# Kernel tuning notes

Hardware: AMD Instinct MI355X
Metric: run time of the kernel (lower is better)

The kernel has to match this reference:

```python
import jax, jax.numpy as jnp
import numpy as np

B, NODES, IN_DIM, OUT_DIM, CAPS, K, NUM_ROUTE = 32, 512, 256, 128, 16, 5, 3

def squash(s):
    # s: [..., out]; scale = |s|^2/(1+|s|^2), direction s/(|s|+eps)
    sn = jnp.sum(s * s, axis=-1, keepdims=True)
    return (sn / (1.0 + sn)) * s / (jnp.sqrt(sn) + 1e-8)

def setup_inputs() -> dict:
    key = jax.random.key(0)
    k1, k2, k3, k4 = jax.random.split(key, 4)
    return {
        "x": jax.random.normal(k1, (B, NODES, IN_DIM), jnp.float32),
        "contribution": jax.random.normal(k2, (B, NODES), jnp.float32),
        "W": jax.random.normal(k3, (K, IN_DIM, OUT_DIM), jnp.float32),
        "alpha": jax.random.normal(k4, (NODES, CAPS, K), jnp.float32),
    }

def reference(x, contribution, W, alpha):
    # per-node, per-capsule transform: sum_k alpha[n,c,k] * W[k,i,o] -> [nodes, caps, in, out]
    Wn = jnp.einsum('nck,kio->ncio', alpha, W)
    # prediction vectors u_hat: [B, caps, nodes, out]
    u_hat = jnp.einsum('bni,ncio->bcno', x, Wn)
    u_det = jax.lax.stop_gradient(u_hat)
    # routing logits b init from (detached) contribution: [B, caps, nodes, 1]
    b = jnp.broadcast_to(
        jax.lax.stop_gradient(contribution)[:, None, :, None],
        (x.shape[0], CAPS, x.shape[1], 1))
    for _ in range(NUM_ROUTE):
        c = jax.nn.softmax(b, axis=1)              # over capsule axis
        v = squash(jnp.sum(c * u_det, axis=2))     # [B, caps, out]
        b = b + jnp.einsum('bcno,bco->bcn', u_det, v)[..., None]
    c = jax.nn.softmax(b, axis=1)
    s = jnp.sum(c * u_hat, axis=2)                 # [B, caps, out] (non-detached)
    return squash(s)
```

## Files before the change

### kernel.cpp

```cpp
#include <hip/hip_runtime.h>
#include <math.h>

#define B_ 32
#define NODES_ 512
#define IN_ 256
#define OUT_ 128
#define CAPS_ 16
#define KW_ 5
#define M_ (B_*NODES_)
#define N_ (KW_*OUT_)
#define NCH 32

typedef __attribute__((ext_vector_type(8))) short short8;
typedef __attribute__((ext_vector_type(4))) float f32x4;

#define Y_BOFF   0
#define L_BOFF   41943040
#define V_BOFF   42991616
#define SP_BOFF  43253760
#define BT_SZ    (N_*IN_*2)

#define YPAD 648
#define APAD 84

__device__ __forceinline__ float b2f(unsigned short u) {
  union { unsigned int i; float f; } c; c.i = ((unsigned int)u) << 16; return c.f;
}
__device__ __forceinline__ unsigned short f2b(float f) {
  union { float f; unsigned int i; } c; c.f = f;
  unsigned int u = c.i;
  u += 0x7fffu + ((u >> 16) & 1u);
  return (unsigned short)(u >> 16);
}
__device__ __forceinline__ void async_load16(const void* g, void* l) {
  __builtin_amdgcn_global_load_lds(
      (const __attribute__((address_space(1))) unsigned int*)g,
      (__attribute__((address_space(3))) unsigned int*)l, 16, 0, 0);
}

__global__ __launch_bounds__(256) void conv_w(const float* __restrict__ W,
                                              unsigned short* __restrict__ bThi,
                                              unsigned short* __restrict__ bTlo) {
  int n = blockIdx.x;
  int i = threadIdx.x;
  int k = n >> 7, o = n & 127;
  float v = W[((size_t)k*IN_ + i)*OUT_ + o];
  unsigned short h = f2b(v);
  size_t dst = ((size_t)(i >> 3)*N_ + n)*8 + (i & 7);
  bThi[dst] = h;
  bTlo[dst] = f2b(v - b2f(h));
}

__global__ __launch_bounds__(512) void gemm_fn(const float* __restrict__ x,
                                               const unsigned short* __restrict__ bThi,
                                               const unsigned short* __restrict__ bTlo,
                                               float* __restrict__ y) {
  __shared__ float A_lds[8*64*4];
  __shared__ short Bh_lds[4*640*8];
  __shared__ short Bl_lds[4*640*8];
  const int t    = threadIdx.x;
  const int w    = t >> 6;
  const int lane = t & 63;
  const int lrow = lane & 15;
  const int lk   = lane >> 4;
  const int m0   = blockIdx.x * 64;
  const int wn0  = w * 80;
  const int arow = t >> 3;
  const int ac4  = t & 7;

  f32x4 acc[4][5];
  #pragma unroll
  for (int i=0;i<4;++i)
    #pragma unroll
    for (int j=0;j<5;++j) acc[i][j] = (f32x4){0.f,0.f,0.f,0.f};

  for (int kbi = 0; kbi < 8; ++kbi) {
    const int kb = kbi*32;
    const unsigned short* bh_src = bThi + (size_t)kbi*4*N_*8;
    const unsigned short* bl_src = bTlo + (size_t)kbi*4*N_*8;
    #pragma unroll
    for (int q=0; q<5; ++q) {
      int db = q*512 + w*64;
      async_load16(bh_src + (size_t)(db + lane)*8, &Bh_lds[db*8]);
      async_load16(bl_src + (size_t)(db + lane)*8, &Bl_lds[db*8]);
    }
    {
      float4 av = *(const float4*)(x + (size_t)(m0 + arow)*IN_ + kb + ac4*4);
      *(float4*)&A_lds[((ac4*64) + arow)*4] = av;
    }
    __syncthreads();

    short8 ah[4], al[4];
    #pragma unroll
    for (int mi=0; mi<4; ++mi) {
      int row = mi*16 + lrow;
      f32x4 a0 = *(const f32x4*)&A_lds[((2*lk  )*64 + row)*4];
      f32x4 a1 = *(const f32x4*)&A_lds[((2*lk+1)*64 + row)*4];
      #pragma unroll
      for (int j=0; j<8; ++j) {
        float f = (j < 4) ? a0[j] : a1[j-4];
        unsigned short h = f2b(f);
        ah[mi][j] = (short)h;
        al[mi][j] = (short)f2b(f - b2f(h));
      }
    }
    #pragma unroll
    for (int ni=0; ni<5; ++ni) {
      int nb = wn0 + ni*16 + lrow;
      short8 bh = *(const short8*)&Bh_lds[(lk*N_ + nb)*8];
      short8 bl = *(const short8*)&Bl_lds[(lk*N_ + nb)*8];
      #pragma unroll
      for (int mi=0; mi<4; ++mi) {
        acc[mi][ni] = __builtin_amdgcn_mfma_f32_16x16x32_bf16(bh, ah[mi], acc[mi][ni], 0, 0, 0);
        acc[mi][ni] = __builtin_amdgcn_mfma_f32_16x16x32_bf16(bh, al[mi], acc[mi][ni], 0, 0, 0);
        acc[mi][ni] = __builtin_amdgcn_mfma_f32_16x16x32_bf16(bl, ah[mi], acc[mi][ni], 0, 0, 0);
      }
    }
    __syncthreads();
  }

  #pragma unroll
  for (int mi=0; mi<4; ++mi) {
    int m = m0 + mi*16 + lrow;
    #pragma unroll
    for (int ni=0; ni<5; ++ni) {
      int nb = wn0 + ni*16 + lk*4;
      float4 o = {acc[mi][ni][0], acc[mi][ni][1], acc[mi][ni][2], acc[mi][ni][3]};
      *(float4*)(y + (size_t)m*N_ + nb) = o;
    }
  }
}

__global__ __launch_bounds__(256) void route_step(const float* __restrict__ y,
                                                  const float* __restrict__ alpha,
                                                  const float* __restrict__ contrib,
                                                  float* __restrict__ logits,
                                                  const float* __restrict__ vin,
                                                  float* __restrict__ s_part,
                                                  int mode) {
  __shared__ __align__(16) float sh_y[16*YPAD];
  __shared__ __align__(16) float sh_v[16*132];
  __shared__ __align__(16) float sh_alpha[16*APAD];
  __shared__ float sh_logit[16][16];

  const int t  = threadIdx.x;
  const int ch = blockIdx.x;
  const int b  = blockIdx.y;
  const int n0 = ch*16;

  const float* ybase = y + ((size_t)(b*NODES_ + n0))*N_;
  float4 yst[10];
  #pragma unroll
  for (int q=0; q<10; ++q) yst[q] = *(const float4*)(ybase + (size_t)(t + q*256)*4);
  #pragma unroll
  for (int q=0; q<10; ++q) {
    int flat = (t + q*256)*4;
    int nd   = flat / 640;
    int rem  = flat - nd*640;
    *(float4*)&sh_y[nd*YPAD + rem] = yst[q];
  }
  const float* abase = alpha + (size_t)n0*CAPS_*KW_;
  for (int i = t; i < 320; i += 256) {
    float4 av = *(const float4*)(abase + i*4);
    int flat = i*4;
    int nd   = flat / 80;
    int rem  = flat - nd*80;
    *(float4*)&sh_alpha[nd*APAD + rem] = av;
  }
  if (mode >= 1) {
    const float* vbase = vin + (size_t)b*CAPS_*OUT_;
    #pragma unroll
    for (int q=0; q<2; ++q) {
      int flat = (t + q*256)*4;
      int c = flat >> 7, o = flat & 127;
      float4 vv = *(const float4*)(vbase + flat);
      *(float4*)&sh_v[c*132 + o] = vv;
    }
    int nd = t & 15, cap = t >> 4;
    sh_logit[nd][cap] = logits[((size_t)b*CAPS_ + cap)*NODES_ + n0 + nd];
  } else {
    int nd = t >> 4, cap = t & 15;
    logits[((size_t)b*CAPS_ + cap)*NODES_ + n0 + nd] = contrib[(size_t)b*NODES_ + n0 + nd];
  }
  __syncthreads();

  if (mode >= 1) {
    const int node = t >> 4, s = t & 15;
    float ar[16][5];
    #pragma unroll
    for (int c=0;c<16;++c)
      #pragma unroll
      for (int k=0;k<5;++k) ar[c][k] = sh_alpha[node*APAD + c*5 + k];
    float acc16[16];
    #pragma unroll
    for (int c=0;c<16;++c) acc16[c] = 0.f;
    const float* yb = &sh_y[node*YPAD];
    #pragma unroll
    for (int j=0;j<8;++j) {
      int o = s + 16*j;
      float y0=yb[o], y1=yb[128+o], y2=yb[256+o], y3=yb[384+o], y4=yb[512+o];
      #pragma unroll
      for (int c=0;c<16;++c) {
        float u = ar[c][0]*y0 + ar[c][1]*y1 + ar[c][2]*y2 + ar[c][3]*y3 + ar[c][4]*y4;
        acc16[c] += u * sh_v[c*132 + o];
      }
    }
    #pragma unroll
    for (int c=0;c<16;++c) {
      acc16[c] += __shfl_xor(acc16[c], 1, 64);
      acc16[c] += __shfl_xor(acc16[c], 2, 64);
      acc16[c] += __shfl_xor(acc16[c], 4, 64);
      acc16[c] += __shfl_xor(acc16[c], 8, 64);
    }
    float mine = 0.f;
    #pragma unroll
    for (int c=0;c<16;++c) mine = (s == c) ? acc16[c] : mine;
    float newl = sh_logit[node][s] + mine;
    sh_logit[node][s] = newl;
    logits[((size_t)b*CAPS_ + s)*NODES_ + n0 + node] = newl;
    __syncthreads();
    if (t < 16) {
      int nd = t;
      float m = -1e30f;
      #pragma unroll
      for (int c=0;c<16;++c) m = fmaxf(m, sh_logit[nd][c]);
      float ssum = 0.f;
      float e[16];
      #pragma unroll
      for (int c=0;c<16;++c) { e[c] = __expf(sh_logit[nd][c]-m); ssum += e[c]; }
      float inv = 1.f/ssum;
      #pragma unroll
      for (int c=0;c<16;++c) sh_logit[nd][c] = e[c]*inv;
    }
  } else {
    int nd = t >> 4, cap = t & 15;
    sh_logit[nd][cap] = 1.f/16.f;
  }
  __syncthreads();

  float* spb = s_part + ((size_t)(b*NCH + ch))*CAPS_*OUT_;
  #pragma unroll
  for (int sl=0; sl<2; ++sl) {
    int slot = t + sl*256;
    int c  = slot & 15;
    int o  = (slot >> 4) * 4;
    float4 acc = {0.f,0.f,0.f,0.f};
    #pragma unroll 4
    for (int nd=0; nd<16; ++nd) {
      const float* al = &sh_alpha[nd*APAD + c*5];
      float a0=al[0],a1=al[1],a2=al[2],a3=al[3],a4=al[4];
      const float* yb = &sh_y[nd*YPAD + o];
      float4 y0 = *(const float4*)(yb);
      float4 y1 = *(const float4*)(yb + 128);
      float4 y2 = *(const float4*)(yb + 256);
      float4 y3 = *(const float4*)(yb + 384);
      float4 y4 = *(const float4*)(yb + 512);
      float cw = sh_logit[nd][c];
      acc.x += cw*(a0*y0.x + a1*y1.x + a2*y2.x + a3*y3.x + a4*y4.x);
      acc.y += cw*(a0*y0.y + a1*y1.y + a2*y2.y + a3*y3.y + a4*y4.y);
      acc.z += cw*(a0*y0.z + a1*y1.z + a2*y2.z + a3*y3.z + a4*y4.z);
      acc.w += cw*(a0*y0.w + a1*y1.w + a2*y2.w + a3*y3.w + a4*y4.w);
    }
    *(float4*)(spb + c*OUT_ + o) = acc;
  }
}

__global__ __launch_bounds__(128) void squash_k(const float* __restrict__ s_part,
                                                float* __restrict__ out) {
  const int bc = blockIdx.x;
  const int o  = threadIdx.x;
  const int b = bc >> 4, c = bc & 15;
  const float* sp = s_part + ((size_t)(b*NCH)*CAPS_ + c)*OUT_ + o;
  float s = 0.f;
  #pragma unroll
  for (int ch=0; ch<NCH; ++ch) s += sp[(size_t)ch*CAPS_*OUT_];
  float ss = s*s;
  #pragma unroll
  for (int off=32; off>0; off>>=1) ss += __shfl_down(ss, off, 64);
  __shared__ float red[2];
  if ((o & 63) == 0) red[o>>6] = ss;
  __syncthreads();
  float sn = red[0] + red[1];
  float scale = (sn/(1.f+sn)) / (sqrtf(sn)+1e-8f);
  out[(size_t)bc*OUT_ + o] = scale*s;
}

extern "C" void kernel_launch(void* const* d_in, const int* in_sizes, int n_in,
                              void* d_out, int out_size, void* d_ws, size_t ws_size,
                              hipStream_t stream) {
  const float* x       = (const float*)d_in[0];
  const float* contrib = (const float*)d_in[1];
  const float* W       = (const float*)d_in[2];
  const float* alpha   = (const float*)d_in[3];
  float* out = (float*)d_out;
  char*  wsb = (char*)d_ws;

  float* y             = (float*)(wsb + Y_BOFF);
  float* logits        = (float*)(wsb + L_BOFF);
  float* v             = (float*)(wsb + V_BOFF);
  float* s_part        = (float*)(wsb + SP_BOFF);
  unsigned short* bThi = (unsigned short*)(wsb + SP_BOFF);
  unsigned short* bTlo = (unsigned short*)(wsb + SP_BOFF + BT_SZ);

  conv_w<<<N_, 256, 0, stream>>>(W, bThi, bTlo);
  gemm_fn<<<M_/64, 512, 0, stream>>>(x, bThi, bTlo, y);

  route_step<<<dim3(NCH, B_), 256, 0, stream>>>(y, alpha, contrib, logits, v, s_part, 0);
  squash_k<<<B_*CAPS_, 128, 0, stream>>>(s_part, v);

  for (int it=0; it<3; ++it) {
    route_step<<<dim3(NCH, B_), 256, 0, stream>>>(y, alpha, contrib, logits, v, s_part, 1);
    squash_k<<<B_*CAPS_, 128, 0, stream>>>(s_part, (it==2) ? out : v);
  }
}
```

Baseline: 151.4 us.

## Restructure routing kernel with transposed alpha, shuffle softmax, register-tiled s accumulation

The routing kernel now stores alpha transposed as [k][c] and computes the agreement term by first dotting y_k with v_c and then combining with alpha, which cuts the FLOPs per node. The per-node softmax runs fully in registers with cross-lane shuffles instead of a 16-thread serial pass through shared memory. The weighted sum over nodes precomputes c*alpha, accumulates an 8x4 register tile per thread, and reduces partials through shared memory by reusing the y buffer. This adds extra barriers and a reduction stage in exchange for fewer LDS reads and fewer FLOPs per output.

```diff
diff --git a/kernel.cpp b/kernel.cpp
--- a/kernel.cpp
+++ b/kernel.cpp
@@ -21,7 +21,6 @@
 #define BT_SZ    (N_*IN_*2)
 
 #define YPAD 648
-#define APAD 84
 
 __device__ __forceinline__ float b2f(unsigned short u) {
   union { unsigned int i; float f; } c; c.i = ((unsigned int)u) << 16; return c.f;
@@ -131,17 +130,18 @@
   }
 }
 
-__global__ __launch_bounds__(256) void route_step(const float* __restrict__ y,
-                                                  const float* __restrict__ alpha,
-                                                  const float* __restrict__ contrib,
-                                                  float* __restrict__ logits,
-                                                  const float* __restrict__ vin,
-                                                  float* __restrict__ s_part,
-                                                  int mode) {
+__global__ __launch_bounds__(256) void route_rs(const float* __restrict__ y,
+                                                const float* __restrict__ alpha,
+                                                const float* __restrict__ contrib,
+                                                float* __restrict__ logits,
+                                                const float* __restrict__ vin,
+                                                float* __restrict__ s_part,
+                                                int mode) {
   __shared__ __align__(16) float sh_y[16*YPAD];
   __shared__ __align__(16) float sh_v[16*132];
-  __shared__ __align__(16) float sh_alpha[16*APAD];
-  __shared__ float sh_logit[16][16];
+  __shared__ __align__(16) float sh_aT[16*80];
+  __shared__ __align__(16) float sh_cwa[16*80];
+  __shared__ float sh_cw[256];
 
   const int t  = threadIdx.x;
   const int ch = blockIdx.x;
@@ -165,7 +165,13 @@
     int flat = i*4;
     int nd   = flat / 80;
     int rem  = flat - nd*80;
-    *(float4*)&sh_alpha[nd*APAD + rem] = av;
+    #pragma unroll
+    for (int e=0; e<4; ++e) {
+      int r = rem + e;
+      int c = r / 5;
+      int k = r - c*5;
+      sh_aT[nd*80 + k*16 + c] = av[e];
+    }
   }
   if (mode >= 1) {
     const float* vbase = vin + (size_t)b*CAPS_*OUT_;
@@ -176,92 +182,128 @@
       float4 vv = *(const float4*)(vbase + flat);
       *(float4*)&sh_v[c*132 + o] = vv;
     }
-    int nd = t & 15, cap = t >> 4;
-    sh_logit[nd][cap] = logits[((size_t)b*CAPS_ + cap)*NODES_ + n0 + nd];
   } else {
-    int nd = t >> 4, cap = t & 15;
-    logits[((size_t)b*CAPS_ + cap)*NODES_ + n0 + nd] = contrib[(size_t)b*NODES_ + n0 + nd];
+    sh_cw[t] = 0.0625f;
+    int nd = t >> 4, c = t & 15;
+    logits[((size_t)b*CAPS_ + c)*NODES_ + n0 + nd] = contrib[(size_t)b*NODES_ + n0 + nd];
   }
   __syncthreads();
 
   if (mode >= 1) {
-    const int node = t >> 4, s = t & 15;
-    float ar[16][5];
-    #pragma unroll
-    for (int c=0;c<16;++c)
-      #pragma unroll
-      for (int k=0;k<5;++k) ar[c][k] = sh_alpha[node*APAD + c*5 + k];
-    float acc16[16];
-    #pragma unroll
-    for (int c=0;c<16;++c) acc16[c] = 0.f;
-    const float* yb = &sh_y[node*YPAD];
+    const int nd = t >> 4, og = t & 15;
+    float4 yq[5][2];
+    #pragma unroll
+    for (int k=0; k<5; ++k) {
+      yq[k][0] = *(const float4*)&sh_y[nd*YPAD + k*128 + og*8];
+      yq[k][1] = *(const float4*)&sh_y[nd*YPAD + k*128 + og*8 + 4];
+    }
+    float p[16];
+    #pragma unroll
+    for (int c=0;c<16;++c) p[c] = 0.f;
+    #pragma unroll
+    for (int cq=0; cq<4; ++cq) {
+      float4 a5[5];
+      #pragma unroll
+      for (int k=0;k<5;++k) a5[k] = *(const float4*)&sh_aT[nd*80 + k*16 + cq*4];
+      #pragma unroll
+      for (int cl=0; cl<4; ++cl) {
+        int c = cq*4 + cl;
+        float4 v0 = *(const float4*)&sh_v[c*132 + og*8];
+        float4 v1 = *(const float4*)&sh_v[c*132 + og*8 + 4];
+        float d[5];
+        #pragma unroll
+        for (int k=0;k<5;++k) {
+          d[k] = yq[k][0].x*v0.x + yq[k][0].y*v0.y + yq[k][0].z*v0.z + yq[k][0].w*v0.w
+               + yq[k][1].x*v1.x + yq[k][1].y*v1.y + yq[k][1].z*v1.z + yq[k][1].w*v1.w;
+        }
+        p[c] += a5[0][cl]*d[0] + a5[1][cl]*d[1] + a5[2][cl]*d[2]
+              + a5[3][cl]*d[3] + a5[4][cl]*d[4];
+      }
+    }
+    #pragma unroll
+    for (int c=0;c<16;++c) {
+      p[c] += __shfl_xor(p[c], 1, 64);
+      p[c] += __shfl_xor(p[c], 2, 64);
+      p[c] += __shfl_xor(p[c], 4, 64);
+      p[c] += __shfl_xor(p[c], 8, 64);
+    }
+    float mine = 0.f;
+    #pragma unroll
+    for (int c=0;c<16;++c) mine = (og == c) ? p[c] : mine;
+    float lold = logits[((size_t)b*CAPS_ + og)*NODES_ + n0 + nd];
+    float newl = lold + mine;
+    logits[((size_t)b*CAPS_ + og)*NODES_ + n0 + nd] = newl;
+    float m = newl;
+    m = fmaxf(m, __shfl_xor(m, 1, 64));
+    m = fmaxf(m, __shfl_xor(m, 2, 64));
+    m = fmaxf(m, __shfl_xor(m, 4, 64));
+    m = fmaxf(m, __shfl_xor(m, 8, 64));
+    float e = __expf(newl - m);
+    float ssum = e;
+    ssum += __shfl_xor(ssum, 1, 64);
+    ssum += __shfl_xor(ssum, 2, 64);
+    ssum += __shfl_xor(ssum, 4, 64);
+    ssum += __shfl_xor(ssum, 8, 64);
+    sh_cw[nd*16 + og] = e / ssum;
+  }
+  __syncthreads();
+
+  #pragma unroll
+  for (int i = t; i < 1280; i += 256) {
+    int nd = i / 80;
+    int c  = i & 15;
+    sh_cwa[i] = sh_cw[nd*16 + c] * sh_aT[i];
+  }
+  __syncthreads();
+
+  {
+    const int oq = t & 31;
+    const int cg = (t >> 5) & 1;
+    const int ng = t >> 6;
+    float acc[8][4];
+    #pragma unroll
+    for (int j=0;j<8;++j)
+      #pragma unroll
+      for (int oo=0;oo<4;++oo) acc[j][oo] = 0.f;
+
+    #pragma unroll
+    for (int ii=0; ii<4; ++ii) {
+      int nd = ng + ii*4;
+      #pragma unroll
+      for (int k=0; k<5; ++k) {
+        float4 yq  = *(const float4*)&sh_y[nd*YPAD + k*128 + oq*4];
+        float4 ca0 = *(const float4*)&sh_cwa[nd*80 + k*16 + cg*8];
+        float4 ca1 = *(const float4*)&sh_cwa[nd*80 + k*16 + cg*8 + 4];
+        float cav[8] = {ca0.x,ca0.y,ca0.z,ca0.w,ca1.x,ca1.y,ca1.z,ca1.w};
+        float yv[4]  = {yq.x,yq.y,yq.z,yq.w};
+        #pragma unroll
+        for (int j=0;j<8;++j)
+          #pragma unroll
+          for (int oo=0;oo<4;++oo)
+            acc[j][oo] += cav[j]*yv[oo];
+      }
+    }
+    __syncthreads();
+    float* red = sh_y;
     #pragma unroll
     for (int j=0;j<8;++j) {
-      int o = s + 16*j;
-      float y0=yb[o], y1=yb[128+o], y2=yb[256+o], y3=yb[384+o], y4=yb[512+o];
-      #pragma unroll
-      for (int c=0;c<16;++c) {
-        float u = ar[c][0]*y0 + ar[c][1]*y1 + ar[c][2]*y2 + ar[c][3]*y3 + ar[c][4]*y4;
-        acc16[c] += u * sh_v[c*132 + o];
-      }
-    }
-    #pragma unroll
-    for (int c=0;c<16;++c) {
-      acc16[c] += __shfl_xor(acc16[c], 1, 64);
-      acc16[c] += __shfl_xor(acc16[c], 2, 64);
-      acc16[c] += __shfl_xor(acc16[c], 4, 64);
-      acc16[c] += __shfl_xor(acc16[c], 8, 64);
-    }
-    float mine = 0.f;
-    #pragma unroll
-    for (int c=0;c<16;++c) mine = (s == c) ? acc16[c] : mine;
-    float newl = sh_logit[node][s] + mine;
-    sh_logit[node][s] = newl;
-    logits[((size_t)b*CAPS_ + s)*NODES_ + n0 + node] = newl;
+      float4 w4 = {acc[j][0], acc[j][1], acc[j][2], acc[j][3]};
+      *(float4*)&red[(size_t)ng*2048 + (cg*8 + j)*128 + oq*4] = w4;
+    }
     __syncthreads();
-    if (t < 16) {
-      int nd = t;
-      float m = -1e30f;
-      #pragma unroll
-      for (int c=0;c<16;++c) m = fmaxf(m, sh_logit[nd][c]);
-      float ssum = 0.f;
-      float e[16];
-      #pragma unroll
-      for (int c=0;c<16;++c) { e[c] = __expf(sh_logit[nd][c]-m); ssum += e[c]; }
-      float inv = 1.f/ssum;
-      #pragma unroll
-      for (int c=0;c<16;++c) sh_logit[nd][c] = e[c]*inv;
-    }
-  } else {
-    int nd = t >> 4, cap = t & 15;
-    sh_logit[nd][cap] = 1.f/16.f;
-  }
-  __syncthreads();
-
-  float* spb = s_part + ((size_t)(b*NCH + ch))*CAPS_*OUT_;
-  #pragma unroll
-  for (int sl=0; sl<2; ++sl) {
-    int slot = t + sl*256;
-    int c  = slot & 15;
-    int o  = (slot >> 4) * 4;
-    float4 acc = {0.f,0.f,0.f,0.f};
-    #pragma unroll 4
-    for (int nd=0; nd<16; ++nd) {
-      const float* al = &sh_alpha[nd*APAD + c*5];
-      float a0=al[0],a1=al[1],a2=al[2],a3=al[3],a4=al[4];
-      const float* yb = &sh_y[nd*YPAD + o];
-      float4 y0 = *(const float4*)(yb);
-      float4 y1 = *(const float4*)(yb + 128);
-      float4 y2 = *(const float4*)(yb + 256);
-      float4 y3 = *(const float4*)(yb + 384);
-      float4 y4 = *(const float4*)(yb + 512);
-      float cw = sh_logit[nd][c];
-      acc.x += cw*(a0*y0.x + a1*y1.x + a2*y2.x + a3*y3.x + a4*y4.x);
-      acc.y += cw*(a0*y0.y + a1*y1.y + a2*y2.y + a3*y3.y + a4*y4.y);
-      acc.z += cw*(a0*y0.z + a1*y1.z + a2*y2.z + a3*y3.z + a4*y4.z);
-      acc.w += cw*(a0*y0.w + a1*y1.w + a2*y2.w + a3*y3.w + a4*y4.w);
-    }
-    *(float4*)(spb + c*OUT_ + o) = acc;
+    const int c2 = t >> 4;
+    const int o2 = (t & 15) * 8;
+    float4 r0 = {0,0,0,0}, r1 = {0,0,0,0};
+    #pragma unroll
+    for (int g=0; g<4; ++g) {
+      float4 q0 = *(const float4*)&red[(size_t)g*2048 + c2*128 + o2];
+      float4 q1 = *(const float4*)&red[(size_t)g*2048 + c2*128 + o2 + 4];
+      r0.x += q0.x; r0.y += q0.y; r0.z += q0.z; r0.w += q0.w;
+      r1.x += q1.x; r1.y += q1.y; r1.z += q1.z; r1.w += q1.w;
+    }
+    float* spb = s_part + ((size_t)(b*NCH + ch)*CAPS_ + c2)*OUT_ + o2;
+    *(float4*)(spb)     = r0;
+    *(float4*)(spb + 4) = r1;
   }
 }
 
@@ -305,11 +347,11 @@
   conv_w<<<N_, 256, 0, stream>>>(W, bThi, bTlo);
   gemm_fn<<<M_/64, 512, 0, stream>>>(x, bThi, bTlo, y);
 
-  route_step<<<dim3(NCH, B_), 256, 0, stream>>>(y, alpha, contrib, logits, v, s_part, 0);
+  route_rs<<<dim3(NCH, B_), 256, 0, stream>>>(y, alpha, contrib, logits, v, s_part, 0);
   squash_k<<<B_*CAPS_, 128, 0, stream>>>(s_part, v);
 
   for (int it=0; it<3; ++it) {
-    route_step<<<dim3(NCH, B_), 256, 0, stream>>>(y, alpha, contrib, logits, v, s_part, 1);
+    route_rs<<<dim3(NCH, B_), 256, 0, stream>>>(y, alpha, contrib, logits, v, s_part, 1);
     squash_k<<<B_*CAPS_, 128, 0, stream>>>(s_part, (it==2) ? out : v);
   }
 }
```

New measurement: 137.9 us. -9.0%, faster.
